# Optimization experiments

Measured on AMD Instinct MI355X. Metric: run time of the kernel, lower is better.

The kernel has to match this reference:

```python
import jax, jax.numpy as jnp
import numpy as np

N = 100000
E = 1600000
D_IN = 128
H = 128
C = 3
EPS_BN = 1e-5
EPS_LN = 1e-5


def _gcn_conv(x, W, b, src, dst, ew, n):
    # PyG GCNConv: x' = D^{-1/2} (A + I) D^{-1/2} (x W) + b, self-loop weight 1
    x = x @ W
    loop = jnp.arange(n)
    src2 = jnp.concatenate([src, loop])
    dst2 = jnp.concatenate([dst, loop])
    ew2 = jnp.concatenate([ew, jnp.ones((n,), dtype=x.dtype)])
    deg = jax.ops.segment_sum(ew2, dst2, num_segments=n)
    dinv = jnp.where(deg > 0, jax.lax.rsqrt(jnp.maximum(deg, 1e-12)), 0.0)
    norm = dinv[src2] * ew2 * dinv[dst2]  # [E+N]
    msgs = x[src2] * norm[:, None]        # [E+N, H] gathered messages
    out = jax.ops.segment_sum(msgs, dst2, num_segments=n)
    return out + b


def setup_inputs() -> dict:
    key = jax.random.key(0)
    ks = jax.random.split(key, 16)
    def lin(k, i, o):
        s = 1.0 / np.sqrt(i)
        k1, k2 = jax.random.split(k)
        return (jax.random.uniform(k1, (i, o), jnp.float32, -s, s),
                jax.random.uniform(k2, (o,), jnp.float32, -s, s))
    x = jax.random.normal(ks[0], (N, D_IN), jnp.float32)
    edge_index = jax.random.randint(ks[1], (2, E), 0, N, jnp.int64)
    edge_attr = jax.random.uniform(ks[2], (E, 1), jnp.float32)
    W_pre, b_pre = lin(ks[3], D_IN, H)
    W1, b1 = lin(ks[4], H, H)
    W2, b2 = lin(ks[5], H, H)
    Wc1, bc1 = lin(ks[6], H, H)
    Wc2, bc2 = lin(ks[7], H, C)
    return {
        "x": x, "edge_index": edge_index, "edge_attr": edge_attr,
        "W_pre": W_pre, "b_pre": b_pre,
        "bn_gamma": jnp.ones((H,), jnp.float32), "bn_beta": jnp.zeros((H,), jnp.float32),
        "bn_mean": jnp.zeros((H,), jnp.float32), "bn_var": jnp.ones((H,), jnp.float32),
        "W1": W1, "b1": b1, "W2": W2, "b2": b2,
        "Wc1": Wc1, "bc1": bc1,
        "ln_g": jnp.ones((H,), jnp.float32), "ln_b": jnp.zeros((H,), jnp.float32),
        "Wc2": Wc2, "bc2": bc2,
    }


def reference(x, edge_index, edge_attr, W_pre, b_pre, bn_gamma, bn_beta, bn_mean, bn_var,
              W1, b1, W2, b2, Wc1, bc1, ln_g, ln_b, Wc2, bc2):
    src, dst = edge_index[0], edge_index[1]
    ew = edge_attr.squeeze()
    n = x.shape[0]
    # input_preprocess: Linear -> BatchNorm1d (eval: running stats) -> ReLU (dropout=identity)
    h = x @ W_pre + b_pre
    h = (h - bn_mean) * jax.lax.rsqrt(bn_var + EPS_BN) * bn_gamma + bn_beta
    h = jax.nn.relu(h)
    residual = h
    # conv layer 1 (+ ReLU, dropout identity in eval)
    h = jax.nn.relu(_gcn_conv(h, W1, b1, src, dst, ew, n))
    # conv layer 2 (last: no activation)
    h = _gcn_conv(h, W2, b2, src, dst, ew, n)
    h = h + residual  # shapes match
    # classifier: Linear -> LayerNorm -> ReLU -> (dropout) -> Linear
    z = h @ Wc1 + bc1
    mu = jnp.mean(z, axis=-1, keepdims=True)
    var = jnp.mean((z - mu) ** 2, axis=-1, keepdims=True)
    z = (z - mu) * jax.lax.rsqrt(var + EPS_LN) * ln_g + ln_b
    z = jax.nn.relu(z)
    return z @ Wc2 + bc2
```

## Files before the change

### kernel.cpp

```cpp
#include <hip/hip_runtime.h>
#include <hip/hip_bf16.h>

typedef __bf16 bf16_t;
typedef bf16_t bf16x8 __attribute__((ext_vector_type(8)));
typedef bf16_t bf16x4 __attribute__((ext_vector_type(4)));
typedef float f32x4 __attribute__((ext_vector_type(4)));
typedef float f32x2 __attribute__((ext_vector_type(2)));

#define EPS_BN 1e-5f
#define EPS_LN 1e-5f
#define SLOTS 32
#define WSCALE 32767.f
#define WINV (1.f / 32767.f)

__device__ __forceinline__ float blo(unsigned u) { return __uint_as_float(u << 16); }
__device__ __forceinline__ float bhi(unsigned u) { return __uint_as_float(u & 0xFFFF0000u); }
__device__ __forceinline__ f32x2 f8lo(unsigned u) { return __builtin_amdgcn_cvt_pk_f32_fp8((int)u, false); }
__device__ __forceinline__ f32x2 f8hi(unsigned u) { return __builtin_amdgcn_cvt_pk_f32_fp8((int)u, true); }


__global__ void prepK(const float* __restrict__ W0, const float* __restrict__ W1,
                      const float* __restrict__ W2, const float* __restrict__ W3,
                      bf16_t* __restrict__ WT, int* __restrict__ cnt,
                      int* __restrict__ ovCnt, int n) {
    int flat = blockIdx.x * 256 + threadIdx.x;
    if (flat < n) cnt[flat] = 0;
    if (flat == 0) *ovCnt = 0;
    if (flat < 65536) {
        int which = flat >> 14, r = flat & 16383;
        const float* W = (which == 0) ? W0 : (which == 1) ? W1 : (which == 2) ? W2 : W3;
        int i = r >> 7, o = r & 127;
        WT[which * 128 * 136 + o * 136 + i] = (bf16_t)W[r];
    }
}


__global__ __launch_bounds__(256) void fillXcdK(
    const int* __restrict__ ei, const float* __restrict__ ea,
    int* __restrict__ cnt, unsigned* __restrict__ slots,
    uint2* __restrict__ ov, int* __restrict__ ovCnt, int E, int range)
{
    int pass = blockIdx.x & 7;
    int blk = blockIdx.x >> 3;
    int e = blk * 256 + threadIdx.x;
    if (e >= E) return;
    int d = ei[E + e];
    int lo = pass * range;
    if (d - lo < 0 || d - lo >= range) return;
    int s = ei[e];
    unsigned wq = __float2uint_rn(ea[e] * WSCALE);
    unsigned pk = ((unsigned)s << 15) | wq;
    int pos = atomicAdd(&cnt[d], 1);
    if (pos < SLOTS) {
        slots[(d << 5) + pos] = pk;
    } else {
        int o = atomicAdd(ovCnt, 1);
        ov[o] = make_uint2((unsigned)d, pk);
    }
}

__global__ __launch_bounds__(256) void degDinvK(
    unsigned* __restrict__ slots, const int* __restrict__ cnt,
    const uint2* __restrict__ ov, const int* __restrict__ ovCnt,
    float* __restrict__ dinv, int n)
{
    int tid = threadIdx.x;
    int node = blockIdx.x * 8 + (tid >> 5);
    int hl = tid & 31;
    if (node >= n) return;
    int c = min(cnt[node], SLOTS);
    int c8 = (c + 7) & ~7;
    float w = 0.f;
    if (hl < c) w = (float)(slots[(node << 5) + hl] & 32767u) * WINV;
    if (hl >= c && hl < c8) slots[(node << 5) + hl] = (unsigned)node << 15;
    for (int off = 1; off < 32; off <<= 1) w += __shfl_xor(w, off);
    int no = *ovCnt;
    for (int k = 0; k < no; ++k) {
        uint2 o = ov[k];
        if ((int)o.x == node) w += (float)(o.y & 32767u) * WINV;
    }
    if (hl == 0) dinv[node] = rsqrtf(fmaxf(1.f + w, 1e-12f));
}


template <int MODE, typename AT>
__global__ __launch_bounds__(256) void gemm128K(
    const AT* __restrict__ A, const bf16_t* __restrict__ WT,
    bf16_t* __restrict__ outb, unsigned* __restrict__ out8,
    const float* __restrict__ colBias,
    const float* __restrict__ bnMean, const float* __restrict__ bnVar,
    const float* __restrict__ bnG, const float* __restrict__ bnB,
    const float* __restrict__ dinv, int nrows)
{
    __shared__ __align__(16) bf16_t Bs[128 * 136];
    int tid = threadIdx.x;
    int rb = blockIdx.x * 64;

    {
        const uint4* src = (const uint4*)WT;
        uint4* dst = (uint4*)Bs;
        if (MODE == 1) {
            for (int i = tid; i < 128 * 17; i += 256) {
                int row = i / 17, k = i - row * 17;
                int so = ((row & 15) << 3) | (row >> 4);
                dst[row * 17 + k] = src[so * 17 + k];
            }
        } else {
            for (int i = tid; i < 128 * 17; i += 256) dst[i] = src[i];
        }
    }

    int lane = tid & 63;
    int wid = tid >> 6;
    int m = lane & 15, q = lane >> 4;
    int myRow = rb + wid * 16 + m;
    int rowL = min(myRow, nrows - 1);

    bf16x8 af[4];
    if constexpr (sizeof(AT) == 4) {
#pragma unroll
        for (int kk = 0; kk < 4; ++kk) {
            float4 v0 = ((const float4*)A)[rowL * 32 + q * 2 + kk * 8];
            float4 v1 = ((const float4*)A)[rowL * 32 + q * 2 + kk * 8 + 1];
            bf16x8 w8;
            w8[0] = (bf16_t)v0.x; w8[1] = (bf16_t)v0.y; w8[2] = (bf16_t)v0.z; w8[3] = (bf16_t)v0.w;
            w8[4] = (bf16_t)v1.x; w8[5] = (bf16_t)v1.y; w8[6] = (bf16_t)v1.z; w8[7] = (bf16_t)v1.w;
            af[kk] = w8;
        }
    } else {
#pragma unroll
        for (int kk = 0; kk < 4; ++kk)
            af[kk] = ((const bf16x8*)A)[rowL * 16 + q + kk * 4];
    }

    __syncthreads();

    f32x4 acc[8];
#pragma unroll
    for (int c = 0; c < 8; ++c) acc[c] = (f32x4){0.f, 0.f, 0.f, 0.f};

#pragma unroll
    for (int kk = 0; kk < 4; ++kk) {
#pragma unroll
        for (int c = 0; c < 8; ++c) {
            bf16x8 bfr = *(const bf16x8*)&Bs[(c * 16 + m) * 136 + q * 8 + kk * 32];
            acc[c] = __builtin_amdgcn_mfma_f32_16x16x32_bf16(af[kk], bfr, acc[c], 0, 0, 0);
        }
    }

    int r0 = rb + wid * 16 + q * 4;
    if (MODE == 1) {
        float dv[4];
#pragma unroll
        for (int i = 0; i < 4; ++i) dv[i] = (r0 + i < nrows) ? dinv[r0 + i] : 0.f;
#pragma unroll
        for (int i = 0; i < 4; ++i) {
            int r = r0 + i;
            if (r < nrows) {
                float v0 = acc[0][i] * dv[i], v1 = acc[1][i] * dv[i];
                float v2 = acc[2][i] * dv[i], v3 = acc[3][i] * dv[i];
                float v4 = acc[4][i] * dv[i], v5 = acc[5][i] * dv[i];
                float v6 = acc[6][i] * dv[i], v7 = acc[7][i] * dv[i];
                int lo = __builtin_amdgcn_cvt_pk_fp8_f32(v0, v1, 0, false);
                lo = __builtin_amdgcn_cvt_pk_fp8_f32(v2, v3, lo, true);
                int hi = __builtin_amdgcn_cvt_pk_fp8_f32(v4, v5, 0, false);
                hi = __builtin_amdgcn_cvt_pk_fp8_f32(v6, v7, hi, true);
                ((uint2*)out8)[(r << 4) | m] = make_uint2((unsigned)lo, (unsigned)hi);
            }
        }
    } else {
#pragma unroll
        for (int c = 0; c < 8; ++c) {
            int j = c * 16 + m;
            float cb = colBias[j];
            float rs = rsqrtf(bnVar[j] + EPS_BN);
            float scale = bnG[j] * rs;
            float shift = bnB[j] - bnMean[j] * scale;
#pragma unroll
            for (int i = 0; i < 4; ++i) {
                int r = r0 + i;
                if (r < nrows) {
                    float v = (acc[c][i] + cb) * scale + shift;
                    outb[r * 128 + j] = (bf16_t)fmaxf(v, 0.f);
                }
            }
        }
    }
}


template <int RELU, int RES>
__global__ __launch_bounds__(256) void aggK(
    const uint4* __restrict__ ts16, const unsigned* __restrict__ slots,
    const int* __restrict__ cnt, const float* __restrict__ dinv,
    const float4* __restrict__ bias, const uint4* __restrict__ residual,
    uint4* __restrict__ out,
    const uint2* __restrict__ ov, const int* __restrict__ ovCnt, int n)
{
    int tid = threadIdx.x;
    int node = blockIdx.x * 8 + (tid >> 5);
    int hl = tid & 31;
    int hb = tid & 32;
    if (node >= n) return;
    int slot = hl >> 3;
    int f = hl & 7;
    int nb = node << 5;

    int c8 = (min(cnt[node], SLOTS) + 7) & ~7;
    unsigned my = slots[nb | hl];
    float myw = (float)(my & 32767u) * WINV;
    int myoff = (int)(my >> 15) << 3;

    f32x2 acc[8];
#pragma unroll
    for (int k = 0; k < 8; ++k) acc[k] = (f32x2){0.f, 0.f};

    if (slot == 1) {
        uint4 su = ts16[(node << 3) + f];
        acc[0] += f8lo(su.x); acc[1] += f8hi(su.x);
        acc[2] += f8lo(su.y); acc[3] += f8hi(su.y);
        acc[4] += f8lo(su.z); acc[5] += f8hi(su.z);
        acc[6] += f8lo(su.w); acc[7] += f8hi(su.w);
    }

    for (int j = 0; j < c8; j += 8) {
        int s0 = hb + j + slot;
        int s1 = s0 + 4;
        int o0 = __shfl(myoff, s0);
        int o1 = __shfl(myoff, s1);
        float w0 = __shfl(myw, s0);
        float w1 = __shfl(myw, s1);
        uint4 u0 = ts16[o0 + f];
        uint4 u1 = ts16[o1 + f];
        f32x2 W0 = (f32x2){w0, w0}, W1 = (f32x2){w1, w1};
        acc[0] += W0 * f8lo(u0.x) + W1 * f8lo(u1.x);
        acc[1] += W0 * f8hi(u0.x) + W1 * f8hi(u1.x);
        acc[2] += W0 * f8lo(u0.y) + W1 * f8lo(u1.y);
        acc[3] += W0 * f8hi(u0.y) + W1 * f8hi(u1.y);
        acc[4] += W0 * f8lo(u0.z) + W1 * f8lo(u1.z);
        acc[5] += W0 * f8hi(u0.z) + W1 * f8hi(u1.z);
        acc[6] += W0 * f8lo(u0.w) + W1 * f8lo(u1.w);
        acc[7] += W0 * f8hi(u0.w) + W1 * f8hi(u1.w);
    }

    int no = *ovCnt;
    for (int k = 0; k < no; ++k) {
        uint2 o = ov[k];
        if ((int)o.x == node && slot == 0) {
            uint4 u = ts16[((int)(o.y >> 15) << 3) + f];
            float w = (float)(o.y & 32767u) * WINV;
            f32x2 W = (f32x2){w, w};
            acc[0] += W * f8lo(u.x); acc[1] += W * f8hi(u.x);
            acc[2] += W * f8lo(u.y); acc[3] += W * f8hi(u.y);
            acc[4] += W * f8lo(u.z); acc[5] += W * f8hi(u.z);
            acc[6] += W * f8lo(u.w); acc[7] += W * f8hi(u.w);
        }
    }

#pragma unroll
    for (int k = 0; k < 8; ++k) {
        f32x2 t;
        t.x = __shfl_xor(acc[k].x, 8);  t.y = __shfl_xor(acc[k].y, 8);
        acc[k] += t;
        t.x = __shfl_xor(acc[k].x, 16); t.y = __shfl_xor(acc[k].y, 16);
        acc[k] += t;
    }

    if (slot == 0) {
        float di = dinv[node];
        float r[16];
#pragma unroll
        for (int k = 0; k < 8; ++k) {
            float4 bb = bias[f * 4 + (k >> 1)];
            float b0 = (k & 1) ? bb.z : bb.x;
            float b1 = (k & 1) ? bb.w : bb.y;
            r[2 * k]     = acc[k].x * di + b0;
            r[2 * k + 1] = acc[k].y * di + b1;
        }
        if (RES) {
            uint4 q0 = residual[(node << 4) + f * 2];
            uint4 q1 = residual[(node << 4) + f * 2 + 1];
            r[0] += blo(q0.x);  r[1] += bhi(q0.x);
            r[2] += blo(q0.y);  r[3] += bhi(q0.y);
            r[4] += blo(q0.z);  r[5] += bhi(q0.z);
            r[6] += blo(q0.w);  r[7] += bhi(q0.w);
            r[8] += blo(q1.x);  r[9] += bhi(q1.x);
            r[10] += blo(q1.y); r[11] += bhi(q1.y);
            r[12] += blo(q1.z); r[13] += bhi(q1.z);
            r[14] += blo(q1.w); r[15] += bhi(q1.w);
        }
        if (RELU) {
#pragma unroll
            for (int k = 0; k < 16; ++k) r[k] = fmaxf(r[k], 0.f);
        }
        bf16x8 o0, o1;
#pragma unroll
        for (int k = 0; k < 8; ++k) { o0[k] = (bf16_t)r[k]; o1[k] = (bf16_t)r[8 + k]; }
        out[(node << 4) + f * 2]     = *(uint4*)&o0;
        out[(node << 4) + f * 2 + 1] = *(uint4*)&o1;
    }
}


__global__ __launch_bounds__(256) void classifierK(
    const bf16_t* __restrict__ A, const bf16_t* __restrict__ WT,
    const float* __restrict__ bc1, const float* __restrict__ g,
    const float* __restrict__ b, const float* __restrict__ Wc2,
    const float* __restrict__ bc2, float* __restrict__ out, int nrows)
{
    __shared__ __align__(16) bf16_t Bs[128 * 136];
    __shared__ float sB[128], sG[128], sLb[128], sW2[384];
    int tid = threadIdx.x;
    int rb = blockIdx.x * 64;

    {
        const uint4* src = (const uint4*)WT;
        uint4* dst = (uint4*)Bs;
        for (int i = tid; i < 128 * 17; i += 256) dst[i] = src[i];
    }
    if (tid < 128) { sB[tid] = bc1[tid]; sG[tid] = g[tid]; sLb[tid] = b[tid]; }
    for (int i = tid; i < 384; i += 256) sW2[i] = Wc2[i];

    int lane = tid & 63;
    int wid = tid >> 6;
    int m = lane & 15, q = lane >> 4;
    int rowL = min(rb + wid * 16 + m, nrows - 1);

    bf16x8 af[4];
#pragma unroll
    for (int kk = 0; kk < 4; ++kk)
        af[kk] = ((const bf16x8*)A)[rowL * 16 + q + kk * 4];

    __syncthreads();

    f32x4 acc[8];
#pragma unroll
    for (int c = 0; c < 8; ++c) acc[c] = (f32x4){0.f, 0.f, 0.f, 0.f};
#pragma unroll
    for (int kk = 0; kk < 4; ++kk) {
#pragma unroll
        for (int c = 0; c < 8; ++c) {
            bf16x8 bfr = *(const bf16x8*)&Bs[(c * 16 + m) * 136 + q * 8 + kk * 32];
            acc[c] = __builtin_amdgcn_mfma_f32_16x16x32_bf16(af[kk], bfr, acc[c], 0, 0, 0);
        }
    }

    int r0 = rb + wid * 16 + q * 4;
#pragma unroll
    for (int i = 0; i < 4; ++i) {
        float s1 = 0.f, s2 = 0.f;
#pragma unroll
        for (int c = 0; c < 8; ++c) {
            float z = acc[c][i] + sB[c * 16 + m];
            acc[c][i] = z;
            s1 += z; s2 += z * z;
        }
#pragma unroll
        for (int off = 1; off < 16; off <<= 1) {
            s1 += __shfl_xor(s1, off);
            s2 += __shfl_xor(s2, off);
        }
        float mu = s1 * (1.f / 128.f);
        float var = s2 * (1.f / 128.f) - mu * mu;
        float rstd = rsqrtf(var + EPS_LN);
        float p0 = 0.f, p1 = 0.f, p2 = 0.f;
#pragma unroll
        for (int c = 0; c < 8; ++c) {
            int j = c * 16 + m;
            float zn = (acc[c][i] - mu) * rstd * sG[j] + sLb[j];
            zn = fmaxf(zn, 0.f);
            p0 += zn * sW2[j * 3 + 0];
            p1 += zn * sW2[j * 3 + 1];
            p2 += zn * sW2[j * 3 + 2];
        }
#pragma unroll
        for (int off = 1; off < 16; off <<= 1) {
            p0 += __shfl_xor(p0, off);
            p1 += __shfl_xor(p1, off);
            p2 += __shfl_xor(p2, off);
        }
        int r = r0 + i;
        if (m == 0 && r < nrows) {
            out[r * 3 + 0] = p0 + bc2[0];
            out[r * 3 + 1] = p1 + bc2[1];
            out[r * 3 + 2] = p2 + bc2[2];
        }
    }
}


extern "C" void kernel_launch(void* const* d_in, const int* in_sizes, int n_in,
                              void* d_out, int out_size, void* d_ws, size_t ws_size,
                              hipStream_t stream) {
    const float* x      = (const float*)d_in[0];
    const int*   ei     = (const int*)d_in[1];
    const float* ea     = (const float*)d_in[2];
    const float* W_pre  = (const float*)d_in[3];
    const float* b_pre  = (const float*)d_in[4];
    const float* bn_g   = (const float*)d_in[5];
    const float* bn_b   = (const float*)d_in[6];
    const float* bn_m   = (const float*)d_in[7];
    const float* bn_v   = (const float*)d_in[8];
    const float* W1     = (const float*)d_in[9];
    const float* b1     = (const float*)d_in[10];
    const float* W2     = (const float*)d_in[11];
    const float* b2     = (const float*)d_in[12];
    const float* Wc1    = (const float*)d_in[13];
    const float* bc1    = (const float*)d_in[14];
    const float* ln_g   = (const float*)d_in[15];
    const float* ln_b   = (const float*)d_in[16];
    const float* Wc2    = (const float*)d_in[17];
    const float* bc2    = (const float*)d_in[18];
    float* outp = (float*)d_out;

    const int N = in_sizes[0] / 128;
    const int E = in_sizes[2];

    char* p = (char*)d_ws;
    auto alloc = [&](size_t bytes) -> void* {
        void* r = (void*)p;
        p += (bytes + 255) & ~(size_t)255;
        return r;
    };
    bf16_t*   h0    = (bf16_t*)alloc((size_t)N * 128 * 2);
    bf16_t*   bufB  = (bf16_t*)alloc((size_t)N * 128 * 2);
    unsigned* ts8   = (unsigned*)alloc((size_t)N * 128);
    float*    dinv  = (float*)alloc((size_t)N * 4);
    int*      cnt   = (int*)alloc((size_t)N * 4);
    int*      ovCnt = (int*)alloc(256);
    uint2*    ov    = (uint2*)alloc((size_t)4096 * 8);
    unsigned* slots = (unsigned*)alloc((size_t)N * SLOTS * 4);
    bf16_t*   WT    = (bf16_t*)alloc((size_t)4 * 128 * 136 * 2);

    bf16_t* WT_pre = WT + 0 * 128 * 136;
    bf16_t* WT_1   = WT + 1 * 128 * 136;
    bf16_t* WT_2   = WT + 2 * 128 * 136;
    bf16_t* WT_c1  = WT + 3 * 128 * 136;

    int gE = (E + 255) / 256;
    int gG = (N + 63) / 64;
    int gH = (N + 7) / 8;
    int gP = (max(N, 65536) + 255) / 256;
    int range = (N + 7) / 8;

    prepK<<<gP, 256, 0, stream>>>(W_pre, W1, W2, Wc1, WT, cnt, ovCnt, N);
    fillXcdK<<<8 * gE, 256, 0, stream>>>(ei, ea, cnt, slots, ov, ovCnt, E, range);
    degDinvK<<<gH, 256, 0, stream>>>(slots, cnt, ov, ovCnt, dinv, N);

    gemm128K<0, float><<<gG, 256, 0, stream>>>(x, WT_pre, h0, nullptr, b_pre, bn_m, bn_v, bn_g, bn_b, nullptr, N);
    gemm128K<1, bf16_t><<<gG, 256, 0, stream>>>(h0, WT_1, nullptr, ts8, nullptr, nullptr, nullptr, nullptr, nullptr, dinv, N);
    aggK<1, 0><<<gH, 256, 0, stream>>>((const uint4*)ts8, slots, cnt, dinv, (const float4*)b1,
                                       nullptr, (uint4*)bufB, ov, ovCnt, N);
    gemm128K<1, bf16_t><<<gG, 256, 0, stream>>>(bufB, WT_2, nullptr, ts8, nullptr, nullptr, nullptr, nullptr, nullptr, dinv, N);
    aggK<0, 1><<<gH, 256, 0, stream>>>((const uint4*)ts8, slots, cnt, dinv, (const float4*)b2,
                                       (const uint4*)h0, (uint4*)bufB, ov, ovCnt, N);
    classifierK<<<gG, 256, 0, stream>>>(bufB, WT_c1, bc1, ln_g, ln_b, Wc2, bc2, outp, N);
}
```

Before: 383.0 us.

## Replace 8-pass edge fill with single-pass bucketing plus per-bucket scatter

The old fill kernel launched eight passes over all edges, each keeping only the destinations in one node range, so the edge list was read eight times. The new bucketK reads edges once and appends packed (dst, src|weight) pairs into eight per-range buckets, using shared-memory counters and one global atomic per bucket per block. scatterK then processes each bucket with blocks interleaved across the low bits of blockIdx, as before, to keep slot atomics localized. This adds one kernel launch and a write and read of an intermediate buffer of about E×8 bytes, plus an overflow path for when a bucket exceeds its capacity.

Result: slower. 417.3 us (+9.0%).

```diff
diff --git a/kernel.cpp b/kernel.cpp
--- a/kernel.cpp
+++ b/kernel.cpp
@@ -22,10 +22,11 @@
 __global__ void prepK(const float* __restrict__ W0, const float* __restrict__ W1,
                       const float* __restrict__ W2, const float* __restrict__ W3,
                       bf16_t* __restrict__ WT, int* __restrict__ cnt,
-                      int* __restrict__ ovCnt, int n) {
+                      int* __restrict__ ovCnt, int* __restrict__ bCnt, int n) {
     int flat = blockIdx.x * 256 + threadIdx.x;
     if (flat < n) cnt[flat] = 0;
     if (flat == 0) *ovCnt = 0;
+    if (flat < 128) bCnt[flat] = 0;
     if (flat < 65536) {
         int which = flat >> 14, r = flat & 16383;
         const float* W = (which == 0) ? W0 : (which == 1) ? W1 : (which == 2) ? W2 : W3;
@@ -35,27 +36,75 @@
 }
 
 
-__global__ __launch_bounds__(256) void fillXcdK(
+__global__ __launch_bounds__(256) void bucketK(
     const int* __restrict__ ei, const float* __restrict__ ea,
+    uint2* __restrict__ bbuf, int* __restrict__ bCnt,
     int* __restrict__ cnt, unsigned* __restrict__ slots,
-    uint2* __restrict__ ov, int* __restrict__ ovCnt, int E, int range)
+    uint2* __restrict__ ov, int* __restrict__ ovCnt,
+    int E, int range, int cap)
+{
+    __shared__ int lcnt[8];
+    __shared__ int lbase[8];
+    int tid = threadIdx.x;
+    if (tid < 8) lcnt[tid] = 0;
+    __syncthreads();
+
+    int e0 = blockIdx.x * 1024 + tid;
+    int d[4]; unsigned pk[4]; int b[4]; int p[4];
+#pragma unroll
+    for (int i = 0; i < 4; ++i) {
+        int e = e0 + i * 256;
+        b[i] = -1;
+        if (e < E) {
+            d[i] = ei[E + e];
+            int s = ei[e];
+            unsigned wq = __float2uint_rn(ea[e] * WSCALE);
+            pk[i] = ((unsigned)s << 15) | wq;
+            b[i] = (int)((unsigned)d[i] / (unsigned)range);
+            p[i] = atomicAdd(&lcnt[b[i]], 1);
+        }
+    }
+    __syncthreads();
+    if (tid < 8) lbase[tid] = atomicAdd(&bCnt[tid * 16], lcnt[tid]);
+    __syncthreads();
+#pragma unroll
+    for (int i = 0; i < 4; ++i) {
+        if (b[i] >= 0) {
+            int idx = lbase[b[i]] + p[i];
+            if (idx < cap) {
+                bbuf[(size_t)b[i] * cap + idx] = make_uint2((unsigned)d[i], pk[i]);
+            } else {
+                int pos = atomicAdd(&cnt[d[i]], 1);
+                if (pos < SLOTS) {
+                    slots[(d[i] << 5) + pos] = pk[i];
+                } else {
+                    int o = atomicAdd(ovCnt, 1);
+                    ov[o] = make_uint2((unsigned)d[i], pk[i]);
+                }
+            }
+        }
+    }
+}
+
+
+__global__ __launch_bounds__(256) void scatterK(
+    const uint2* __restrict__ bbuf, const int* __restrict__ bCnt,
+    int* __restrict__ cnt, unsigned* __restrict__ slots,
+    uint2* __restrict__ ov, int* __restrict__ ovCnt, int cap, int gS)
 {
     int pass = blockIdx.x & 7;
-    int blk = blockIdx.x >> 3;
-    int e = blk * 256 + threadIdx.x;
-    if (e >= E) return;
-    int d = ei[E + e];
-    int lo = pass * range;
-    if (d - lo < 0 || d - lo >= range) return;
-    int s = ei[e];
-    unsigned wq = __float2uint_rn(ea[e] * WSCALE);
-    unsigned pk = ((unsigned)s << 15) | wq;
-    int pos = atomicAdd(&cnt[d], 1);
-    if (pos < SLOTS) {
-        slots[(d << 5) + pos] = pk;
-    } else {
-        int o = atomicAdd(ovCnt, 1);
-        ov[o] = make_uint2((unsigned)d, pk);
+    int nb = min(bCnt[pass * 16], cap);
+    const uint2* buf = bbuf + (size_t)pass * cap;
+    for (int i = (blockIdx.x >> 3) * 256 + threadIdx.x; i < nb; i += gS * 256) {
+        uint2 u = buf[i];
+        int d = (int)u.x;
+        int pos = atomicAdd(&cnt[d], 1);
+        if (pos < SLOTS) {
+            slots[(d << 5) + pos] = u.y;
+        } else {
+            int o = atomicAdd(ovCnt, 1);
+            ov[o] = u;
+        }
     }
 }
 
@@ -431,20 +480,25 @@
     uint2*    ov    = (uint2*)alloc((size_t)4096 * 8);
     unsigned* slots = (unsigned*)alloc((size_t)N * SLOTS * 4);
     bf16_t*   WT    = (bf16_t*)alloc((size_t)4 * 128 * 136 * 2);
+    int       cap   = E / 8 + 16384;
+    uint2*    bbuf  = (uint2*)alloc((size_t)8 * cap * 8);
+    int*      bCnt  = (int*)alloc(512);
 
     bf16_t* WT_pre = WT + 0 * 128 * 136;
     bf16_t* WT_1   = WT + 1 * 128 * 136;
     bf16_t* WT_2   = WT + 2 * 128 * 136;
     bf16_t* WT_c1  = WT + 3 * 128 * 136;
 
-    int gE = (E + 255) / 256;
     int gG = (N + 63) / 64;
     int gH = (N + 7) / 8;
     int gP = (max(N, 65536) + 255) / 256;
     int range = (N + 7) / 8;
-
-    prepK<<<gP, 256, 0, stream>>>(W_pre, W1, W2, Wc1, WT, cnt, ovCnt, N);
-    fillXcdK<<<8 * gE, 256, 0, stream>>>(ei, ea, cnt, slots, ov, ovCnt, E, range);
+    int gB = (E + 1023) / 1024;
+    int gS = (E / 8 + 255) / 256 + 2;
+
+    prepK<<<gP, 256, 0, stream>>>(W_pre, W1, W2, Wc1, WT, cnt, ovCnt, bCnt, N);
+    bucketK<<<gB, 256, 0, stream>>>(ei, ea, bbuf, bCnt, cnt, slots, ov, ovCnt, E, range, cap);
+    scatterK<<<8 * gS, 256, 0, stream>>>(bbuf, bCnt, cnt, slots, ov, ovCnt, cap, gS);
     degDinvK<<<gH, 256, 0, stream>>>(slots, cnt, ov, ovCnt, dinv, N);
 
     gemm128K<0, float><<<gG, 256, 0, stream>>>(x, WT_pre, h0, nullptr, b_pre, bn_m, bn_v, bn_g, bn_b, nullptr, N);
```

## Replace atomic slot fill with two-pass bucket binning and LDS-built adjacency

Applied to the files above, without the earlier changes.

Replaces the 8-pass XCD-partitioned global-atomic edge fill and the separate degree kernel with two kernels. The first bins edges into destination-node buckets using LDS counters and one global atomic per bucket per block. The second builds each bucket's 32-slot adjacency, degree sums and dinv in shared memory and writes them out coalesced. The aim is to cut scattered global atomics and the 8x rereads of the edge list, at the cost of an intermediate bucket buffer, extra overflow paths and larger overflow capacities.

After: 322.4 us. 15.8% less time.

```diff
diff --git a/kernel.cpp b/kernel.cpp
--- a/kernel.cpp
+++ b/kernel.cpp
@@ -12,6 +12,9 @@
 #define SLOTS 32
 #define WSCALE 32767.f
 #define WINV (1.f / 32767.f)
+#define RNODES 448
+#define OV_CAP 16384
+#define OVA_CAP 65536
 
 __device__ __forceinline__ float blo(unsigned u) { return __uint_as_float(u << 16); }
 __device__ __forceinline__ float bhi(unsigned u) { return __uint_as_float(u & 0xFFFF0000u); }
@@ -21,11 +24,11 @@
 
 __global__ void prepK(const float* __restrict__ W0, const float* __restrict__ W1,
                       const float* __restrict__ W2, const float* __restrict__ W3,
-                      bf16_t* __restrict__ WT, int* __restrict__ cnt,
-                      int* __restrict__ ovCnt, int n) {
+                      bf16_t* __restrict__ WT, int* __restrict__ bCnt,
+                      int* __restrict__ ovCnt, int* __restrict__ ovACnt, int n) {
     int flat = blockIdx.x * 256 + threadIdx.x;
-    if (flat < n) cnt[flat] = 0;
-    if (flat == 0) *ovCnt = 0;
+    if (flat == 0) { *ovCnt = 0; *ovACnt = 0; }
+    if (flat < 4096) bCnt[flat] = 0;
     if (flat < 65536) {
         int which = flat >> 14, r = flat & 16383;
         const float* W = (which == 0) ? W0 : (which == 1) ? W1 : (which == 2) ? W2 : W3;
@@ -35,51 +38,117 @@
 }
 
 
-__global__ __launch_bounds__(256) void fillXcdK(
+__global__ __launch_bounds__(256) void binK(
     const int* __restrict__ ei, const float* __restrict__ ea,
-    int* __restrict__ cnt, unsigned* __restrict__ slots,
-    uint2* __restrict__ ov, int* __restrict__ ovCnt, int E, int range)
+    uint2* __restrict__ bbuf, int* __restrict__ bCnt,
+    uint2* __restrict__ ovA, int* __restrict__ ovACnt,
+    int E, int cap, int nbuck)
 {
-    int pass = blockIdx.x & 7;
-    int blk = blockIdx.x >> 3;
-    int e = blk * 256 + threadIdx.x;
-    if (e >= E) return;
-    int d = ei[E + e];
-    int lo = pass * range;
-    if (d - lo < 0 || d - lo >= range) return;
-    int s = ei[e];
-    unsigned wq = __float2uint_rn(ea[e] * WSCALE);
-    unsigned pk = ((unsigned)s << 15) | wq;
-    int pos = atomicAdd(&cnt[d], 1);
-    if (pos < SLOTS) {
-        slots[(d << 5) + pos] = pk;
-    } else {
-        int o = atomicAdd(ovCnt, 1);
-        ov[o] = make_uint2((unsigned)d, pk);
-    }
-}
-
-__global__ __launch_bounds__(256) void degDinvK(
-    unsigned* __restrict__ slots, const int* __restrict__ cnt,
-    const uint2* __restrict__ ov, const int* __restrict__ ovCnt,
-    float* __restrict__ dinv, int n)
+    __shared__ int lcnt[256];
+    __shared__ int gbase[256];
+    int tid = threadIdx.x;
+    if (tid < nbuck) lcnt[tid] = 0;
+    __syncthreads();
+
+    int e0 = blockIdx.x * 4096 + tid;
+    int d[16]; unsigned pk[16]; int p[16];
+#pragma unroll
+    for (int k = 0; k < 16; ++k) {
+        int e = e0 + k * 256;
+        p[k] = -1;
+        if (e < E) {
+            d[k] = ei[E + e];
+            int s = ei[e];
+            unsigned wq = __float2uint_rn(ea[e] * WSCALE);
+            pk[k] = ((unsigned)s << 15) | wq;
+            p[k] = atomicAdd(&lcnt[(unsigned)d[k] / RNODES], 1);
+        }
+    }
+    __syncthreads();
+    if (tid < nbuck) gbase[tid] = atomicAdd(&bCnt[tid * 16], lcnt[tid]);
+    __syncthreads();
+#pragma unroll
+    for (int k = 0; k < 16; ++k) {
+        if (p[k] >= 0) {
+            int b = (unsigned)d[k] / RNODES;
+            int idx = gbase[b] + p[k];
+            if (idx < cap) {
+                bbuf[(size_t)b * cap + idx] = make_uint2((unsigned)d[k], pk[k]);
+            } else {
+                int o = atomicAdd(ovACnt, 1);
+                if (o < OVA_CAP) ovA[o] = make_uint2((unsigned)d[k], pk[k]);
+            }
+        }
+    }
+}
+
+
+__global__ __launch_bounds__(256) void buildK(
+    const uint2* __restrict__ bbuf, const int* __restrict__ bCnt,
+    const uint2* __restrict__ ovA, const int* __restrict__ ovACnt,
+    unsigned* __restrict__ slots, int* __restrict__ cnt,
+    float* __restrict__ dinv, uint2* __restrict__ ov, int* __restrict__ ovCnt,
+    int cap, int n)
 {
+    __shared__ unsigned slotsL[RNODES * 32];
+    __shared__ int cntL[RNODES];
+    __shared__ float wsumL[RNODES];
     int tid = threadIdx.x;
-    int node = blockIdx.x * 8 + (tid >> 5);
-    int hl = tid & 31;
-    if (node >= n) return;
-    int c = min(cnt[node], SLOTS);
-    int c8 = (c + 7) & ~7;
-    float w = 0.f;
-    if (hl < c) w = (float)(slots[(node << 5) + hl] & 32767u) * WINV;
-    if (hl >= c && hl < c8) slots[(node << 5) + hl] = (unsigned)node << 15;
-    for (int off = 1; off < 32; off <<= 1) w += __shfl_xor(w, off);
-    int no = *ovCnt;
-    for (int k = 0; k < no; ++k) {
-        uint2 o = ov[k];
-        if ((int)o.x == node) w += (float)(o.y & 32767u) * WINV;
-    }
-    if (hl == 0) dinv[node] = rsqrtf(fmaxf(1.f + w, 1e-12f));
+    int base = blockIdx.x * RNODES;
+
+    for (int j = tid; j < RNODES; j += 256) { cntL[j] = 0; wsumL[j] = 0.f; }
+    __syncthreads();
+
+    int nb = min(bCnt[blockIdx.x * 16], cap);
+    const uint2* buf = bbuf + (size_t)blockIdx.x * cap;
+    for (int i = tid; i < nb; i += 256) {
+        uint2 u = buf[i];
+        int local = (int)u.x - base;
+        int pos = atomicAdd(&cntL[local], 1);
+        atomicAdd(&wsumL[local], (float)(u.y & 32767u) * WINV);
+        if (pos < SLOTS) {
+            slotsL[local * 32 + pos] = u.y;
+        } else {
+            int o = atomicAdd(ovCnt, 1);
+            if (o < OV_CAP) ov[o] = u;
+        }
+    }
+    int no = min(*ovACnt, OVA_CAP);
+    for (int k = tid; k < no; k += 256) {
+        uint2 u = ovA[k];
+        int local = (int)u.x - base;
+        if (local >= 0 && local < RNODES) {
+            int pos = atomicAdd(&cntL[local], 1);
+            atomicAdd(&wsumL[local], (float)(u.y & 32767u) * WINV);
+            if (pos < SLOTS) {
+                slotsL[local * 32 + pos] = u.y;
+            } else {
+                int o = atomicAdd(ovCnt, 1);
+                if (o < OV_CAP) ov[o] = u;
+            }
+        }
+    }
+    __syncthreads();
+
+    for (int j = tid; j < RNODES; j += 256) {
+        int node = base + j;
+        if (node < n) {
+            int c = cntL[j];
+            int cm = min(c, SLOTS);
+            int c8 = (cm + 7) & ~7;
+            for (int k2 = cm; k2 < c8; ++k2) slotsL[j * 32 + k2] = (unsigned)node << 15;
+            cnt[node] = c;
+            dinv[node] = rsqrtf(fmaxf(1.f + wsumL[j], 1e-12f));
+        }
+    }
+    __syncthreads();
+
+    int vnodes = min(n - base, RNODES);
+    if (vnodes <= 0) return;
+    const uint4* sl4 = (const uint4*)slotsL;
+    uint4* sg4 = (uint4*)(slots + ((size_t)base << 5));
+    int lim = vnodes * 8;
+    for (int i = tid; i < lim; i += 256) sg4[i] = sl4[i];
 }
 
 
@@ -243,7 +312,7 @@
         acc[7] += W0 * f8hi(u0.w) + W1 * f8hi(u1.w);
     }
 
-    int no = *ovCnt;
+    int no = min(*ovCnt, OV_CAP);
     for (int k = 0; k < no; ++k) {
         uint2 o = ov[k];
         if ((int)o.x == node && slot == 0) {
@@ -428,24 +497,29 @@
     float*    dinv  = (float*)alloc((size_t)N * 4);
     int*      cnt   = (int*)alloc((size_t)N * 4);
     int*      ovCnt = (int*)alloc(256);
-    uint2*    ov    = (uint2*)alloc((size_t)4096 * 8);
+    int*      ovACnt= (int*)alloc(256);
+    uint2*    ov    = (uint2*)alloc((size_t)OV_CAP * 8);
+    uint2*    ovA   = (uint2*)alloc((size_t)OVA_CAP * 8);
     unsigned* slots = (unsigned*)alloc((size_t)N * SLOTS * 4);
     bf16_t*   WT    = (bf16_t*)alloc((size_t)4 * 128 * 136 * 2);
+    int       nbuck = (N + RNODES - 1) / RNODES;
+    int       cap   = E / nbuck + 4096;
+    uint2*    bbuf  = (uint2*)alloc((size_t)nbuck * cap * 8);
+    int*      bCnt  = (int*)alloc(4096 * 4);
 
     bf16_t* WT_pre = WT + 0 * 128 * 136;
     bf16_t* WT_1   = WT + 1 * 128 * 136;
     bf16_t* WT_2   = WT + 2 * 128 * 136;
     bf16_t* WT_c1  = WT + 3 * 128 * 136;
 
-    int gE = (E + 255) / 256;
     int gG = (N + 63) / 64;
     int gH = (N + 7) / 8;
     int gP = (max(N, 65536) + 255) / 256;
-    int range = (N + 7) / 8;
-
-    prepK<<<gP, 256, 0, stream>>>(W_pre, W1, W2, Wc1, WT, cnt, ovCnt, N);
-    fillXcdK<<<8 * gE, 256, 0, stream>>>(ei, ea, cnt, slots, ov, ovCnt, E, range);
-    degDinvK<<<gH, 256, 0, stream>>>(slots, cnt, ov, ovCnt, dinv, N);
+    int gBin = (E + 4095) / 4096;
+
+    prepK<<<gP, 256, 0, stream>>>(W_pre, W1, W2, Wc1, WT, bCnt, ovCnt, ovACnt, N);
+    binK<<<gBin, 256, 0, stream>>>(ei, ea, bbuf, bCnt, ovA, ovACnt, E, cap, nbuck);
+    buildK<<<nbuck, 256, 0, stream>>>(bbuf, bCnt, ovA, ovACnt, slots, cnt, dinv, ov, ovCnt, cap, N);
 
     gemm128K<0, float><<<gG, 256, 0, stream>>>(x, WT_pre, h0, nullptr, b_pre, bn_m, bn_v, bn_g, bn_b, nullptr, N);
     gemm128K<1, bf16_t><<<gG, 256, 0, stream>>>(h0, WT_1, nullptr, ts8, nullptr, nullptr, nullptr, nullptr, nullptr, dinv, N);
```
